# Kernel tuning notes

Hardware: AMD Instinct MI355X
Metric: run time of the kernel (lower is better)

## Reference

```python
import jax, jax.numpy as jnp
import numpy as np

N_QUBITS = 23
DEPTH = 2
ROT_PER_QUBIT = 2
DIM = 1 << N_QUBITS
CYCLE = ('RY', 'RZ', 'RX')
C64 = jnp.complex64


def _rot_mat(kind, theta):
    # standard rotation gates; theta is the full angle, matrices use theta/2
    c = jnp.cos(theta / 2).astype(C64)
    s = jnp.sin(theta / 2).astype(C64)
    if kind == 'RX':
        return jnp.stack([jnp.stack([c, -1j * s]), jnp.stack([-1j * s, c])])
    if kind == 'RY':
        return jnp.stack([jnp.stack([c, -s]), jnp.stack([s, c])])
    # RZ = diag(exp(-i t/2), exp(i t/2))
    z = jnp.zeros((), C64)
    return jnp.stack([jnp.stack([c - 1j * s, z]), jnp.stack([z, c + 1j * s])])


def _apply_1q(psi, mat, q):
    # qubit 0 is the most significant bit -> axis q after factoring
    psi = psi.reshape(1 << q, 2, -1)
    psi = jnp.einsum('ij,ajb->aib', mat, psi)
    return psi.reshape(-1)


def _apply_cnot(psi, c):
    # control c, target c+1 (adjacent): flip target axis where control == 1
    psi = psi.reshape(1 << c, 2, 2, -1)
    psi = jnp.stack([psi[:, 0], psi[:, 1, ::-1]], axis=1)
    return psi.reshape(-1)


def setup_inputs() -> dict:
    key = jax.random.key(0)
    k1, k2, k3 = jax.random.split(key, 3)
    thetas = jax.random.uniform(k1, (DEPTH * N_QUBITS * ROT_PER_QUBIT,), dtype=jnp.float32)
    state_real = jax.random.normal(k2, (DIM,), dtype=jnp.float32)
    state_imag = jax.random.normal(k3, (DIM,), dtype=jnp.float32)
    return {"thetas": thetas, "state_real": state_real, "state_imag": state_imag}


def reference(thetas, state_real, state_imag):
    psi = (state_real + 1j * state_imag).astype(C64)
    psi = psi / jnp.linalg.norm(psi)  # normalized input state
    idx = 0
    for layer in range(DEPTH):
        for q in range(N_QUBITS):
            for r in range(ROT_PER_QUBIT):
                kind = CYCLE[(layer * ROT_PER_QUBIT + r) % 3]
                psi = _apply_1q(psi, _rot_mat(kind, thetas[idx]), q)
                idx += 1
        for q in range(N_QUBITS - 1):
            psi = _apply_cnot(psi, q)
    probs = jnp.abs(psi) ** 2
    # Z on qubit 0 (MSB): eig +1 for first half, -1 for second half
    p = probs.reshape(2, -1)
    return (p[0].sum() - p[1].sum()).astype(jnp.float32)
```

## Files before the change

kernel.cpp:

```cpp
#include <hip/hip_runtime.h>

#define Q21 (1u<<21)
#define THREADS 512
#define BLOCKS 1024


struct cd { double r, i; };
__device__ __forceinline__ cd cmul(cd a, cd b){ return {a.r*b.r - a.i*b.i, a.r*b.i + a.i*b.r}; }
__device__ __forceinline__ cd cjg(cd a){ return {a.r, -a.i}; }
__device__ __forceinline__ cd cadd(cd a, cd b){ return {a.r+b.r, a.i+b.i}; }

__device__ __forceinline__ double psin(double x){
  double x2 = x*x;
  return x*(1.0 + x2*(-1.0/6.0 + x2*(1.0/120.0 + x2*(-1.0/5040.0 + x2*(1.0/362880.0)))));
}
__device__ __forceinline__ double pcos(double x){
  double x2 = x*x;
  return 1.0 + x2*(-0.5 + x2*(1.0/24.0 + x2*(-1.0/720.0 + x2*(1.0/40320.0 + x2*(-1.0/3628800.0)))));
}

__global__ __launch_bounds__(THREADS)
void gramk(const float* __restrict__ sr, const float* __restrict__ si,
           double* __restrict__ part){
  int tid = threadIdx.x;
  int gt = blockIdx.x*THREADS + tid;
  int v  = gt<<2;
  float rr[4][4], ii[4][4];
  *(float4*)&rr[0][0] = *(const float4*)(sr+v);
  *(float4*)&rr[1][0] = *(const float4*)(sr+v+Q21);
  *(float4*)&rr[2][0] = *(const float4*)(sr+v+2*Q21);
  *(float4*)&rr[3][0] = *(const float4*)(sr+v+3*Q21);
  *(float4*)&ii[0][0] = *(const float4*)(si+v);
  *(float4*)&ii[1][0] = *(const float4*)(si+v+Q21);
  *(float4*)&ii[2][0] = *(const float4*)(si+v+2*Q21);
  *(float4*)&ii[3][0] = *(const float4*)(si+v+3*Q21);
  float acc[16];
  #pragma unroll
  for(int k=0;k<16;++k) acc[k]=0.f;
  const int pm[6]={0,0,0,1,1,2}, pn[6]={1,2,3,2,3,3};
  #pragma unroll
  for(int e=0;e<4;++e){
    float qr[4]={rr[0][e],rr[1][e],rr[2][e],rr[3][e]};
    float qi[4]={ii[0][e],ii[1][e],ii[2][e],ii[3][e]};
    #pragma unroll
    for(int m=0;m<4;++m) acc[m] += qr[m]*qr[m] + qi[m]*qi[m];
    #pragma unroll
    for(int p=0;p<6;++p){
      int m=pm[p], n=pn[p];
      acc[4+2*p] += qr[m]*qr[n] + qi[m]*qi[n];
      acc[5+2*p] += qr[m]*qi[n] - qi[m]*qr[n];
    }
  }
  __shared__ float lds[THREADS*16];
  __shared__ double red[256];
  float4* lds4 = (float4*)lds;
  #pragma unroll
  for(int pc=0; pc<4; ++pc){
    int c = pc ^ (tid&3);
    lds4[(tid<<2)|pc] = make_float4(acc[4*c],acc[4*c+1],acc[4*c+2],acc[4*c+3]);
  }
  __syncthreads();
  if(tid<256){
    int comp = tid&15, grp = tid>>4;
    double s = 0.0;
    #pragma unroll
    for(int j=0;j<32;++j){
      int r = (grp<<5)|j;
      s += (double)lds[(r<<4) | (comp ^ ((r&3)<<2))];
    }
    red[tid] = s;
  }
  __syncthreads();
  if(tid<16){
    double s=0;
    #pragma unroll
    for(int g=0; g<16; ++g) s += red[g*16 + tid];
    part[blockIdx.x*16 + tid] = s;
  }
}

__global__ void fink(const float* __restrict__ thetas,
                     const double* __restrict__ part, float* __restrict__ out){
  __shared__ double red[16][17];
  __shared__ double G[16];
  int t = threadIdx.x;
  int comp = t&15, grp = t>>4;
  double s = 0.0;
  #pragma unroll 8
  for(int b=grp; b<BLOCKS; b+=16) s += part[b*16 + comp];
  red[comp][grp] = s;
  __syncthreads();
  if(t<16){
    double g=0;
    #pragma unroll
    for(int i=0;i<16;++i) g += red[t][i];
    G[t]=g;
  }
  __syncthreads();
  if(t==0){
    double a0=0.5*(double)thetas[0], b0=0.5*(double)thetas[1];
    double a1=0.5*(double)thetas[2], b1=0.5*(double)thetas[3];
    double ax=0.5*(double)thetas[46], bx=0.5*(double)thetas[47];
    cd U0[2][2], U1[2][2], V[2][2];
    {
      double ca=pcos(a0), sa=psin(a0), cb=pcos(b0), sb=psin(b0);
      U0[0][0]={ca*cb,-ca*sb}; U0[0][1]={-sa*cb, sa*sb};
      U0[1][0]={sa*cb, sa*sb}; U0[1][1]={ ca*cb, ca*sb};
    }
    {
      double ca=pcos(a1), sa=psin(a1), cb=pcos(b1), sb=psin(b1);
      U1[0][0]={ca*cb,-ca*sb}; U1[0][1]={-sa*cb, sa*sb};
      U1[1][0]={sa*cb, sa*sb}; U1[1][1]={ ca*cb, ca*sb};
    }
    {
      double ca=pcos(ax), sa=psin(ax), cb=pcos(bx), sb=psin(bx);
      V[0][0]={cb*ca, sb*sa}; V[0][1]={-sb*ca,-cb*sa};
      V[1][0]={sb*ca,-cb*sa}; V[1][1]={ cb*ca,-sb*sa};
    }
    double aM = (V[0][0].r*V[0][0].r+V[0][0].i*V[0][0].i)
              - (V[1][0].r*V[1][0].r+V[1][0].i*V[1][0].i);
    cd t1 = cmul(cjg(V[0][0]),V[0][1]), t2 = cmul(cjg(V[1][0]),V[1][1]);
    cd O01 = {t1.r - t2.r, t1.i - t2.i};
    cd O10 = cjg(O01);
    cd W[4][4];
    #pragma unroll
    for(int m=0;m<4;++m)
      #pragma unroll
      for(int n=0;n<4;++n)
        W[m][n] = cmul(U0[m>>1][n>>1], U1[m&1][n&1]);
    const int pm[6]={0,0,0,1,1,2}, pn[6]={1,2,3,2,3,3};
    double num = 0.0;
    #pragma unroll
    for(int e=0;e<10;++e){
      int m = (e<4) ? e : pm[e-4];
      int n = (e<4) ? e : pn[e-4];
      cd c = {0,0};
      #pragma unroll
      for(int j=0;j<4;++j){
        double sgn = (j<2) ? aM : -aM;
        cd term = cmul(cjg(W[j][m]), W[j][n]);
        c.r += sgn*term.r; c.i += sgn*term.i;
      }
      c = cadd(c, cmul(O01, cadd(cmul(cjg(W[0][m]),W[3][n]), cmul(cjg(W[1][m]),W[2][n]))));
      c = cadd(c, cmul(O10, cadd(cmul(cjg(W[3][m]),W[0][n]), cmul(cjg(W[2][m]),W[1][n]))));
      if(e<4) num += c.r * G[e];
      else    num += 2.0*c.r*G[4+2*(e-4)] - 2.0*c.i*G[5+2*(e-4)];
    }
    double den = G[0]+G[1]+G[2]+G[3];
    out[0] = (float)(num/den);
  }
}

extern "C" void kernel_launch(void* const* d_in, const int* in_sizes, int n_in,
                              void* d_out, int out_size, void* d_ws, size_t ws_size,
                              hipStream_t stream){
  (void)in_sizes; (void)n_in; (void)out_size; (void)ws_size;
  const float* thetas = (const float*)d_in[0];
  const float* sr = (const float*)d_in[1];
  const float* si = (const float*)d_in[2];
  double* part = (double*)d_ws;

  gramk<<<BLOCKS, THREADS, 0, stream>>>(sr, si, part);
  fink<<<1, 256, 0, stream>>>(thetas, part, (float*)d_out);
}
```

Before: 105.6 us.

## Transpose partial sums and parallelize finalize kernel with wavefront shuffles

The gram kernel now writes per-block partials component-major, so the finalize kernel can read each component contiguously with double2 loads. The finalize kernel runs with 1024 threads: one wavefront per component reduces via shuffles. The 4x4 W matrix and the 10 coefficient terms are computed in parallel lanes instead of by a single thread. This targets the serial tail latency of the final launch, at the cost of more threads and more synchronisation.

```diff
diff --git a/kernel.cpp b/kernel.cpp
--- a/kernel.cpp
+++ b/kernel.cpp
@@ -75,33 +75,37 @@
     double s=0;
     #pragma unroll
     for(int g=0; g<16; ++g) s += red[g*16 + tid];
-    part[blockIdx.x*16 + tid] = s;
+    part[tid*BLOCKS + blockIdx.x] = s;
   }
 }
 
-__global__ void fink(const float* __restrict__ thetas,
-                     const double* __restrict__ part, float* __restrict__ out){
-  __shared__ double red[16][17];
-  __shared__ double G[16];
+__global__ __launch_bounds__(1024)
+void fink(const float* __restrict__ thetas,
+          const double* __restrict__ part, float* __restrict__ out){
+  __shared__ double Gs[16];
+  __shared__ cd Ws[16];
   int t = threadIdx.x;
-  int comp = t&15, grp = t>>4;
-  double s = 0.0;
-  #pragma unroll 8
-  for(int b=grp; b<BLOCKS; b+=16) s += part[b*16 + comp];
-  red[comp][grp] = s;
-  __syncthreads();
-  if(t<16){
-    double g=0;
+  int comp = t>>6, lane = t&63;
+  {
+    const double2* p2 = (const double2*)(part + comp*BLOCKS);
+    double s = 0.0;
     #pragma unroll
-    for(int i=0;i<16;++i) g += red[t][i];
-    G[t]=g;
+    for(int j=0;j<8;++j){
+      double2 d = p2[lane + 64*j];
+      s += d.x + d.y;
+    }
+    #pragma unroll
+    for(int k=32;k>=1;k>>=1) s += __shfl_down(s, k);
+    if(lane==0) Gs[comp] = s;
   }
   __syncthreads();
-  if(t==0){
+
+  cd U0[2][2], U1[2][2], V[2][2];
+  double aM=0.0; cd O01={0,0}, O10={0,0};
+  if(t<64){
     double a0=0.5*(double)thetas[0], b0=0.5*(double)thetas[1];
     double a1=0.5*(double)thetas[2], b1=0.5*(double)thetas[3];
     double ax=0.5*(double)thetas[46], bx=0.5*(double)thetas[47];
-    cd U0[2][2], U1[2][2], V[2][2];
     {
       double ca=pcos(a0), sa=psin(a0), cb=pcos(b0), sb=psin(b0);
       U0[0][0]={ca*cb,-ca*sb}; U0[0][1]={-sa*cb, sa*sb};
@@ -117,37 +121,45 @@
       V[0][0]={cb*ca, sb*sa}; V[0][1]={-sb*ca,-cb*sa};
       V[1][0]={sb*ca,-cb*sa}; V[1][1]={ cb*ca,-sb*sa};
     }
-    double aM = (V[0][0].r*V[0][0].r+V[0][0].i*V[0][0].i)
-              - (V[1][0].r*V[1][0].r+V[1][0].i*V[1][0].i);
+    aM = (V[0][0].r*V[0][0].r+V[0][0].i*V[0][0].i)
+       - (V[1][0].r*V[1][0].r+V[1][0].i*V[1][0].i);
     cd t1 = cmul(cjg(V[0][0]),V[0][1]), t2 = cmul(cjg(V[1][0]),V[1][1]);
-    cd O01 = {t1.r - t2.r, t1.i - t2.i};
-    cd O10 = cjg(O01);
-    cd W[4][4];
-    #pragma unroll
-    for(int m=0;m<4;++m)
-      #pragma unroll
-      for(int n=0;n<4;++n)
-        W[m][n] = cmul(U0[m>>1][n>>1], U1[m&1][n&1]);
-    const int pm[6]={0,0,0,1,1,2}, pn[6]={1,2,3,2,3,3};
-    double num = 0.0;
-    #pragma unroll
-    for(int e=0;e<10;++e){
-      int m = (e<4) ? e : pm[e-4];
-      int n = (e<4) ? e : pn[e-4];
+    O01 = {t1.r - t2.r, t1.i - t2.i};
+    O10 = cjg(O01);
+    if(t<16){
+      int mm=t>>2, nn=t&3;
+      cd u0 = (mm&2) ? ((nn&2)?U0[1][1]:U0[1][0]) : ((nn&2)?U0[0][1]:U0[0][0]);
+      cd u1 = (mm&1) ? ((nn&1)?U1[1][1]:U1[1][0]) : ((nn&1)?U1[0][1]:U1[0][0]);
+      Ws[t] = cmul(u0,u1);
+    }
+  }
+  __syncthreads();
+  if(t<64){
+    double contrib = 0.0;
+    if(t<10){
+      int p = t-4;
+      int m = (t<4) ? t : ((0x940 >> (2*p)) & 3);
+      int n = (t<4) ? t : ((0xFB9 >> (2*p)) & 3);
       cd c = {0,0};
       #pragma unroll
       for(int j=0;j<4;++j){
         double sgn = (j<2) ? aM : -aM;
-        cd term = cmul(cjg(W[j][m]), W[j][n]);
+        cd term = cmul(cjg(Ws[j*4+m]), Ws[j*4+n]);
         c.r += sgn*term.r; c.i += sgn*term.i;
       }
-      c = cadd(c, cmul(O01, cadd(cmul(cjg(W[0][m]),W[3][n]), cmul(cjg(W[1][m]),W[2][n]))));
-      c = cadd(c, cmul(O10, cadd(cmul(cjg(W[3][m]),W[0][n]), cmul(cjg(W[2][m]),W[1][n]))));
-      if(e<4) num += c.r * G[e];
-      else    num += 2.0*c.r*G[4+2*(e-4)] - 2.0*c.i*G[5+2*(e-4)];
+      c = cadd(c, cmul(O01, cadd(cmul(cjg(Ws[0*4+m]),Ws[3*4+n]),
+                                 cmul(cjg(Ws[1*4+m]),Ws[2*4+n]))));
+      c = cadd(c, cmul(O10, cadd(cmul(cjg(Ws[3*4+m]),Ws[0*4+n]),
+                                 cmul(cjg(Ws[2*4+m]),Ws[1*4+n]))));
+      contrib = (t<4) ? c.r*Gs[t]
+                      : 2.0*c.r*Gs[4+2*p] - 2.0*c.i*Gs[5+2*p];
     }
-    double den = G[0]+G[1]+G[2]+G[3];
-    out[0] = (float)(num/den);
+    #pragma unroll
+    for(int k=8;k>=1;k>>=1) contrib += __shfl_down(contrib, k);
+    if(t==0){
+      double den = Gs[0]+Gs[1]+Gs[2]+Gs[3];
+      out[0] = (float)(contrib/den);
+    }
   }
 }
 
@@ -161,5 +173,5 @@
   double* part = (double*)d_ws;
 
   gramk<<<BLOCKS, THREADS, 0, stream>>>(sr, si, part);
-  fink<<<1, 256, 0, stream>>>(thetas, part, (float*)d_out);
+  fink<<<1, 1024, 0, stream>>>(thetas, part, (float*)d_out);
 }
```

Result: faster. 103.5 us (-2.0%).
